# Kernel optimization log

Measured on AMD Instinct MI355X. Metric: run time of the kernel, lower is better.

Reference implementation:

```python
import jax, jax.numpy as jnp
import numpy as np

KEY_DIM = 32
NUM_HEADS = 4
B, T, F, D = 32, 64, 128, 64


def _proj_in(x, w, b):
    # x: [B,T,F,D], w: [D,H,K], b: [H,K] -> [B,T,F,H,K]
    return jnp.einsum("btfd,dhk->btfhk", x, w) + b


def _axial_mha(x, wq, bq, wk, bk, wv, bv, wo, bo, axis):
    # Keras MultiHeadAttention with attention_axes=(axis,); dropout inactive at inference.
    scale = 1.0 / np.sqrt(KEY_DIM)
    q = _proj_in(x, wq, bq) * scale
    k = _proj_in(x, wk, bk)
    v = _proj_in(x, wv, bv)
    if axis == 1:  # temporal attention, feature axis acts as batch
        scores = jnp.einsum("bqfhk,bsfhk->bfhqs", q, k)  # [B,F,H,Tq,Tk]
        probs = jax.nn.softmax(scores, axis=-1)
        o = jnp.einsum("bfhqs,bsfhk->bqfhk", probs, v)
    else:  # feature attention, temporal axis acts as batch
        scores = jnp.einsum("btqhk,btshk->bthqs", q, k)  # [B,T,H,Fq,Fk]
        probs = jax.nn.softmax(scores, axis=-1)
        o = jnp.einsum("bthqs,btshk->btqhk", probs, v)
    return jnp.einsum("btfhk,hkd->btfd", o, wo) + bo


def setup_inputs() -> dict:
    key = jax.random.key(0)
    ks = jax.random.split(key, 10)
    std = 0.02
    w = lambda k, shape: (jax.random.normal(k, shape, jnp.float32) * std)
    inp = {"x": jax.random.normal(ks[0], (B, T, F, D), jnp.float32)}
    for i, n in enumerate(["tq", "tk", "tv", "fq", "fk", "fv"]):
        inp[n + "_w"] = w(ks[1 + i], (D, NUM_HEADS, KEY_DIM))
        inp[n + "_b"] = jnp.zeros((NUM_HEADS, KEY_DIM), jnp.float32)
    inp["to_w"] = w(ks[7], (NUM_HEADS, KEY_DIM, D))
    inp["to_b"] = jnp.zeros((D,), jnp.float32)
    inp["fo_w"] = w(ks[8], (NUM_HEADS, KEY_DIM, D))
    inp["fo_b"] = jnp.zeros((D,), jnp.float32)
    return inp


def reference(x, tq_w, tq_b, tk_w, tk_b, tv_w, tv_b, to_w, to_b,
              fq_w, fq_b, fk_w, fk_b, fv_w, fv_b, fo_w, fo_b):
    temporal_out = _axial_mha(x, tq_w, tq_b, tk_w, tk_b, tv_w, tv_b, to_w, to_b, axis=1)
    feature_out = _axial_mha(x, fq_w, fq_b, fk_w, fk_b, fv_w, fv_b, fo_w, fo_b, axis=2)
    return temporal_out + feature_out
```

## Files before the change

kernel.cpp:

```cpp
#include <hip/hip_runtime.h>

typedef unsigned short u16;
typedef unsigned int   u32;
typedef short v8s __attribute__((ext_vector_type(8)));
typedef float v4f __attribute__((ext_vector_type(4)));

#define DEV __device__ __forceinline__
#define MFMA(a,b,c) __builtin_amdgcn_mfma_f32_16x16x32_bf16((a),(b),(c),0,0,0)

constexpr int Bb = 32, Tt = 64, Ff = 128, Dd = 64, Hh = 4, Kk = 32;

DEV u16 f2b(float f) {
    u32 u = __float_as_uint(f);
    return (u16)((u + 0x7fffu + ((u >> 16) & 1u)) >> 16);
}

__global__ __launch_bounds__(256)
void prep_weights(const float* __restrict__ tq, const float* __restrict__ tk,
                  const float* __restrict__ tv, const float* __restrict__ fq,
                  const float* __restrict__ fk, const float* __restrict__ fv,
                  const float* __restrict__ to_, const float* __restrict__ fo,
                  u16* __restrict__ ws)
{
    int idx = blockIdx.x * 256 + threadIdx.x;
    if (idx < 49152) {
        int p = idx >> 13, rem = idx & 8191;
        int h = rem >> 11, ch = (rem >> 6) & 31, d = rem & 63;
        const float* w = (p==0)?tq:(p==1)?tk:(p==2)?tv:(p==3)?fq:(p==4)?fk:fv;
        ws[idx] = f2b(w[d*128 + h*32 + ch]);
    } else {
        int i2 = idx - 49152;
        int path = i2 >> 13, rem = i2 & 8191;
        int h = rem >> 11, d = (rem >> 5) & 63, k2 = rem & 31;
        const float* w = path ? fo : to_;
        ws[idx] = f2b(w[h*2048 + k2*64 + d]);
    }
}

template<int NR, int MODE>
__global__ __launch_bounds__(NR*4)
void axial_mfma(const float* __restrict__ x, const u16* __restrict__ wsw,
                const float* __restrict__ bq, const float* __restrict__ bk,
                const float* __restrict__ bv, const float* __restrict__ bo,
                float* __restrict__ out)
{
    constexpr int W   = NR / 16;
    constexpr int NT  = W * 64;
    constexpr int NRp = NR + 8;
    constexpr int o_ql = 0;
    constexpr int o_kl = o_ql + NR * 32;
    constexpr int o_vt = o_kl + NR * 32;
    constexpr int o_pl = o_vt + 32 * NRp;
    constexpr int SMEM = o_pl + NR * NRp;
    __shared__ alignas(16) u16 sm[SMEM];
    (void)NT;

    const int tid  = threadIdx.x;
    const int w    = tid >> 6;
    const int lane = tid & 63;
    const int quad = lane >> 4;
    const int l15  = lane & 15;
    const int bid  = blockIdx.x;

    int base, rstride;
    if (MODE == 0) { int b = bid >> 7, f = bid & 127; base = b*(Tt*Ff*Dd) + f*Dd; rstride = Ff*Dd; }
    else           { base = bid * (Ff*Dd); rstride = Dd; }

    constexpr int PB = (MODE == 0) ? 0 : 3;
    const u16* wql = wsw + (PB+0)*8192;
    const u16* wkl = wsw + (PB+1)*8192;
    const u16* wvl = wsw + (PB+2)*8192;
    const u16* wol = wsw + 49152 + MODE*8192;

    v8s xfrag[2];
#pragma unroll
    for (int ks = 0; ks < 2; ++ks) {
        const float* xp = x + base + (w*16 + l15)*rstride + ks*32 + quad*8;
        float4 a = *reinterpret_cast<const float4*>(xp);
        float4 b = *reinterpret_cast<const float4*>(xp + 4);
        v8s f;
        f[0]=(short)f2b(a.x); f[1]=(short)f2b(a.y); f[2]=(short)f2b(a.z); f[3]=(short)f2b(a.w);
        f[4]=(short)f2b(b.x); f[5]=(short)f2b(b.y); f[6]=(short)f2b(b.z); f[7]=(short)f2b(b.w);
        xfrag[ks] = f;
    }

    v4f outAcc[4];
#pragma unroll
    for (int i = 0; i < 4; ++i) outAcc[i] = (v4f){0.f,0.f,0.f,0.f};

    const float scale = 0.17677669529663687f;
    const v4f vzero = (v4f){0.f,0.f,0.f,0.f};

#pragma unroll 1
    for (int h = 0; h < Hh; ++h) {
        __syncthreads();

        {
            const u16* wb = wql + h*2048;
#pragma unroll
            for (int nt = 0; nt < 2; ++nt) {
                v4f acc = vzero;
#pragma unroll
                for (int ks = 0; ks < 2; ++ks) {
                    v8s wf = *reinterpret_cast<const v8s*>(wb + (nt*16+l15)*64 + ks*32 + quad*8);
                    acc = MFMA(xfrag[ks], wf, acc);
                }
                float bias = bq[h*32 + nt*16 + l15];
#pragma unroll
                for (int r = 0; r < 4; ++r)
                    sm[o_ql + (w*16 + quad*4 + r)*32 + nt*16 + l15] = f2b((acc[r] + bias) * scale);
            }
        }
        {
            const u16* wb = wkl + h*2048;
#pragma unroll
            for (int nt = 0; nt < 2; ++nt) {
                v4f acc = vzero;
#pragma unroll
                for (int ks = 0; ks < 2; ++ks) {
                    v8s wf = *reinterpret_cast<const v8s*>(wb + (nt*16+l15)*64 + ks*32 + quad*8);
                    acc = MFMA(xfrag[ks], wf, acc);
                }
                float bias = bk[h*32 + nt*16 + l15];
#pragma unroll
                for (int r = 0; r < 4; ++r)
                    sm[o_kl + (w*16 + quad*4 + r)*32 + nt*16 + l15] = f2b(acc[r] + bias);
            }
        }
        {
            const u16* wb = wvl + h*2048;
#pragma unroll
            for (int nt = 0; nt < 2; ++nt) {
                v4f acc = vzero;
#pragma unroll
                for (int ks = 0; ks < 2; ++ks) {
                    v8s wf = *reinterpret_cast<const v8s*>(wb + (nt*16+l15)*64 + ks*32 + quad*8);
                    acc = MFMA(xfrag[ks], wf, acc);
                }
                float bias = bv[h*32 + nt*16 + l15];
                u32 lo = (u32)f2b(acc[0]+bias) | ((u32)f2b(acc[1]+bias) << 16);
                u32 hi = (u32)f2b(acc[2]+bias) | ((u32)f2b(acc[3]+bias) << 16);
                int ch = nt*16 + l15;
                *reinterpret_cast<uint2*>(&sm[o_vt + ch*NRp + w*16 + quad*4]) = make_uint2(lo, hi);
            }
        }
        __syncthreads();

        v8s qf = *reinterpret_cast<const v8s*>(&sm[o_ql + (w*16 + l15)*32 + quad*8]);
        v4f S[W];
#pragma unroll
        for (int ct = 0; ct < W; ++ct) {
            v8s kf = *reinterpret_cast<const v8s*>(&sm[o_kl + (ct*16 + l15)*32 + quad*8]);
            S[ct] = MFMA(qf, kf, vzero);
        }
        float mrow[4], rl[4];
#pragma unroll
        for (int r = 0; r < 4; ++r) {
            float mm = S[0][r];
#pragma unroll
            for (int ct = 1; ct < W; ++ct) mm = fmaxf(mm, S[ct][r]);
#pragma unroll
            for (int msk = 1; msk < 16; msk <<= 1) mm = fmaxf(mm, __shfl_xor(mm, msk, 16));
            mrow[r] = mm;
        }
#pragma unroll
        for (int r = 0; r < 4; ++r) {
            float ss = 0.f;
#pragma unroll
            for (int ct = 0; ct < W; ++ct) { float p = __expf(S[ct][r] - mrow[r]); S[ct][r] = p; ss += p; }
#pragma unroll
            for (int msk = 1; msk < 16; msk <<= 1) ss += __shfl_xor(ss, msk, 16);
            rl[r] = 1.f / ss;
        }
#pragma unroll
        for (int ct = 0; ct < W; ++ct)
#pragma unroll
            for (int r = 0; r < 4; ++r)
                sm[o_pl + (w*16 + quad*4 + r)*NRp + ct*16 + l15] = f2b(S[ct][r] * rl[r]);

        v4f Oacc[2] = { vzero, vzero };
#pragma unroll
        for (int ks = 0; ks < NR/32; ++ks) {
            v8s pf = *reinterpret_cast<const v8s*>(&sm[o_pl + (w*16 + l15)*NRp + ks*32 + quad*8]);
#pragma unroll
            for (int nt = 0; nt < 2; ++nt) {
                v8s vf = *reinterpret_cast<const v8s*>(&sm[o_vt + (nt*16 + l15)*NRp + ks*32 + quad*8]);
                Oacc[nt] = MFMA(pf, vf, Oacc[nt]);
            }
        }
#pragma unroll
        for (int nt = 0; nt < 2; ++nt)
#pragma unroll
            for (int r = 0; r < 4; ++r)
                sm[o_ql + (w*16 + quad*4 + r)*32 + nt*16 + l15] = f2b(Oacc[nt][r]);

        v8s of = *reinterpret_cast<const v8s*>(&sm[o_ql + (w*16 + l15)*32 + quad*8]);
        {
            const u16* wb = wol + h*2048;
#pragma unroll
            for (int nt = 0; nt < 4; ++nt) {
                v8s wf = *reinterpret_cast<const v8s*>(wb + (nt*16 + l15)*32 + quad*8);
                outAcc[nt] = MFMA(of, wf, outAcc[nt]);
            }
        }
    }

#pragma unroll
    for (int nt = 0; nt < 4; ++nt) {
        int d = nt*16 + l15;
        float bias = bo[d];
#pragma unroll
        for (int r = 0; r < 4; ++r) {
            int row = w*16 + quad*4 + r;
            float* p = out + base + row*rstride + d;
            float v = outAcc[nt][r] + bias;
            if (MODE == 1) v += *p;
            *p = v;
        }
    }
}

extern "C" void kernel_launch(void* const* d_in, const int* in_sizes, int n_in,
                              void* d_out, int out_size, void* d_ws, size_t ws_size,
                              hipStream_t stream) {
    const float* x   = (const float*)d_in[0];
    const float* tqw = (const float*)d_in[1];  const float* tqb = (const float*)d_in[2];
    const float* tkw = (const float*)d_in[3];  const float* tkb = (const float*)d_in[4];
    const float* tvw = (const float*)d_in[5];  const float* tvb = (const float*)d_in[6];
    const float* fqw = (const float*)d_in[7];  const float* fqb = (const float*)d_in[8];
    const float* fkw = (const float*)d_in[9];  const float* fkb = (const float*)d_in[10];
    const float* fvw = (const float*)d_in[11]; const float* fvb = (const float*)d_in[12];
    const float* tow = (const float*)d_in[13]; const float* tob = (const float*)d_in[14];
    const float* fow = (const float*)d_in[15]; const float* fob = (const float*)d_in[16];
    float* out = (float*)d_out;
    u16* ws = (u16*)d_ws;

    hipLaunchKernelGGL(prep_weights, dim3(256), dim3(256), 0, stream,
                       tqw, tkw, tvw, fqw, fkw, fvw, tow, fow, ws);
    hipLaunchKernelGGL((axial_mfma<64,0>), dim3(Bb*Ff), dim3(256), 0, stream,
                       x, ws, tqb, tkb, tvb, tob, out);
    hipLaunchKernelGGL((axial_mfma<128,1>), dim3(Bb*Tt), dim3(512), 0, stream,
                       x, ws, fqb, fkb, fvb, fob, out);
}
```

Measured before the change: 390.8 us.

## Transpose MFMA operand order for packed stores, row-local softmax, and vectorized output

Swaps the A/B operands of the Q, K, score, PV and output-projection MFMAs so each lane holds four consecutive columns of a single row. This lets the kernel write bf16 pairs with packed 64-bit LDS stores and float4 global stores instead of scalar ones. Softmax now reduces across quads with two cross-lane shuffles instead of four, and the Q/K LDS rows are padded to 40 elements to reduce bank conflicts. It also replaces the round-to-nearest-even bf16 conversion with a cheaper round-half-up packed conversion, which changes rounding slightly.

Result: faster. 381.0 us (-2.5%).

```diff
diff --git a/kernel.cpp b/kernel.cpp
--- a/kernel.cpp
+++ b/kernel.cpp
@@ -13,6 +13,11 @@
 DEV u16 f2b(float f) {
     u32 u = __float_as_uint(f);
     return (u16)((u + 0x7fffu + ((u >> 16) & 1u)) >> 16);
+}
+DEV u32 pk2(float a, float b) {
+    u32 x = __float_as_uint(a) + 0x8000u;
+    u32 y = __float_as_uint(b) + 0x8000u;
+    return (x >> 16) | (y & 0xffff0000u);
 }
 
 __global__ __launch_bounds__(256)
@@ -45,15 +50,14 @@
                 float* __restrict__ out)
 {
     constexpr int W   = NR / 16;
-    constexpr int NT  = W * 64;
+    constexpr int QP  = 40;
     constexpr int NRp = NR + 8;
-    constexpr int o_ql = 0;
-    constexpr int o_kl = o_ql + NR * 32;
-    constexpr int o_vt = o_kl + NR * 32;
-    constexpr int o_pl = o_vt + 32 * NRp;
-    constexpr int SMEM = o_pl + NR * NRp;
+    constexpr int o_q  = 0;
+    constexpr int o_k  = o_q + NR * QP;
+    constexpr int o_vt = o_k + NR * QP;
+    constexpr int o_p  = o_vt + 32 * NRp;
+    constexpr int SMEM = o_p + NR * NRp;
     __shared__ alignas(16) u16 sm[SMEM];
-    (void)NT;
 
     const int tid  = threadIdx.x;
     const int w    = tid >> 6;
@@ -79,8 +83,9 @@
         float4 a = *reinterpret_cast<const float4*>(xp);
         float4 b = *reinterpret_cast<const float4*>(xp + 4);
         v8s f;
-        f[0]=(short)f2b(a.x); f[1]=(short)f2b(a.y); f[2]=(short)f2b(a.z); f[3]=(short)f2b(a.w);
-        f[4]=(short)f2b(b.x); f[5]=(short)f2b(b.y); f[6]=(short)f2b(b.z); f[7]=(short)f2b(b.w);
+        u32* fu = reinterpret_cast<u32*>(&f);
+        fu[0] = pk2(a.x, a.y); fu[1] = pk2(a.z, a.w);
+        fu[2] = pk2(b.x, b.y); fu[3] = pk2(b.z, b.w);
         xfrag[ks] = f;
     }
 
@@ -103,12 +108,12 @@
 #pragma unroll
                 for (int ks = 0; ks < 2; ++ks) {
                     v8s wf = *reinterpret_cast<const v8s*>(wb + (nt*16+l15)*64 + ks*32 + quad*8);
-                    acc = MFMA(xfrag[ks], wf, acc);
+                    acc = MFMA(wf, xfrag[ks], acc);
                 }
-                float bias = bq[h*32 + nt*16 + l15];
-#pragma unroll
-                for (int r = 0; r < 4; ++r)
-                    sm[o_ql + (w*16 + quad*4 + r)*32 + nt*16 + l15] = f2b((acc[r] + bias) * scale);
+                float4 b4 = *reinterpret_cast<const float4*>(bq + h*32 + nt*16 + quad*4);
+                u32 lo = pk2((acc[0]+b4.x)*scale, (acc[1]+b4.y)*scale);
+                u32 hi = pk2((acc[2]+b4.z)*scale, (acc[3]+b4.w)*scale);
+                *reinterpret_cast<uint2*>(&sm[o_q + (w*16+l15)*QP + nt*16 + quad*4]) = make_uint2(lo, hi);
             }
         }
         {
@@ -119,12 +124,12 @@
 #pragma unroll
                 for (int ks = 0; ks < 2; ++ks) {
                     v8s wf = *reinterpret_cast<const v8s*>(wb + (nt*16+l15)*64 + ks*32 + quad*8);
-                    acc = MFMA(xfrag[ks], wf, acc);
+                    acc = MFMA(wf, xfrag[ks], acc);
                 }
-                float bias = bk[h*32 + nt*16 + l15];
-#pragma unroll
-                for (int r = 0; r < 4; ++r)
-                    sm[o_kl + (w*16 + quad*4 + r)*32 + nt*16 + l15] = f2b(acc[r] + bias);
+                float4 b4 = *reinterpret_cast<const float4*>(bk + h*32 + nt*16 + quad*4);
+                u32 lo = pk2(acc[0]+b4.x, acc[1]+b4.y);
+                u32 hi = pk2(acc[2]+b4.z, acc[3]+b4.w);
+                *reinterpret_cast<uint2*>(&sm[o_k + (w*16+l15)*QP + nt*16 + quad*4]) = make_uint2(lo, hi);
             }
         }
         {
@@ -138,85 +143,83 @@
                     acc = MFMA(xfrag[ks], wf, acc);
                 }
                 float bias = bv[h*32 + nt*16 + l15];
-                u32 lo = (u32)f2b(acc[0]+bias) | ((u32)f2b(acc[1]+bias) << 16);
-                u32 hi = (u32)f2b(acc[2]+bias) | ((u32)f2b(acc[3]+bias) << 16);
+                u32 lo = pk2(acc[0]+bias, acc[1]+bias);
+                u32 hi = pk2(acc[2]+bias, acc[3]+bias);
                 int ch = nt*16 + l15;
                 *reinterpret_cast<uint2*>(&sm[o_vt + ch*NRp + w*16 + quad*4]) = make_uint2(lo, hi);
             }
         }
         __syncthreads();
 
-        v8s qf = *reinterpret_cast<const v8s*>(&sm[o_ql + (w*16 + l15)*32 + quad*8]);
+        v8s qf = *reinterpret_cast<const v8s*>(&sm[o_q + (w*16+l15)*QP + quad*8]);
         v4f S[W];
 #pragma unroll
         for (int ct = 0; ct < W; ++ct) {
-            v8s kf = *reinterpret_cast<const v8s*>(&sm[o_kl + (ct*16 + l15)*32 + quad*8]);
-            S[ct] = MFMA(qf, kf, vzero);
-        }
-        float mrow[4], rl[4];
-#pragma unroll
-        for (int r = 0; r < 4; ++r) {
-            float mm = S[0][r];
-#pragma unroll
-            for (int ct = 1; ct < W; ++ct) mm = fmaxf(mm, S[ct][r]);
-#pragma unroll
-            for (int msk = 1; msk < 16; msk <<= 1) mm = fmaxf(mm, __shfl_xor(mm, msk, 16));
-            mrow[r] = mm;
-        }
-#pragma unroll
-        for (int r = 0; r < 4; ++r) {
-            float ss = 0.f;
-#pragma unroll
-            for (int ct = 0; ct < W; ++ct) { float p = __expf(S[ct][r] - mrow[r]); S[ct][r] = p; ss += p; }
-#pragma unroll
-            for (int msk = 1; msk < 16; msk <<= 1) ss += __shfl_xor(ss, msk, 16);
-            rl[r] = 1.f / ss;
-        }
+            v8s kf = *reinterpret_cast<const v8s*>(&sm[o_k + (ct*16+l15)*QP + quad*8]);
+            S[ct] = MFMA(kf, qf, vzero);
+        }
+        float mm = S[0][0];
 #pragma unroll
         for (int ct = 0; ct < W; ++ct)
 #pragma unroll
-            for (int r = 0; r < 4; ++r)
-                sm[o_pl + (w*16 + quad*4 + r)*NRp + ct*16 + l15] = f2b(S[ct][r] * rl[r]);
+            for (int r = 0; r < 4; ++r) mm = fmaxf(mm, S[ct][r]);
+        mm = fmaxf(mm, __shfl_xor(mm, 16));
+        mm = fmaxf(mm, __shfl_xor(mm, 32));
+        float ss = 0.f;
+#pragma unroll
+        for (int ct = 0; ct < W; ++ct)
+#pragma unroll
+            for (int r = 0; r < 4; ++r) { float p = __expf(S[ct][r] - mm); S[ct][r] = p; ss += p; }
+        ss += __shfl_xor(ss, 16);
+        ss += __shfl_xor(ss, 32);
+        float rl = 1.f / ss;
+#pragma unroll
+        for (int ct = 0; ct < W; ++ct) {
+            u32 lo = pk2(S[ct][0]*rl, S[ct][1]*rl);
+            u32 hi = pk2(S[ct][2]*rl, S[ct][3]*rl);
+            *reinterpret_cast<uint2*>(&sm[o_p + (w*16+l15)*NRp + ct*16 + quad*4]) = make_uint2(lo, hi);
+        }
 
         v4f Oacc[2] = { vzero, vzero };
 #pragma unroll
         for (int ks = 0; ks < NR/32; ++ks) {
-            v8s pf = *reinterpret_cast<const v8s*>(&sm[o_pl + (w*16 + l15)*NRp + ks*32 + quad*8]);
-#pragma unroll
-            for (int nt = 0; nt < 2; ++nt) {
-                v8s vf = *reinterpret_cast<const v8s*>(&sm[o_vt + (nt*16 + l15)*NRp + ks*32 + quad*8]);
-                Oacc[nt] = MFMA(pf, vf, Oacc[nt]);
-            }
-        }
-#pragma unroll
-        for (int nt = 0; nt < 2; ++nt)
-#pragma unroll
-            for (int r = 0; r < 4; ++r)
-                sm[o_ql + (w*16 + quad*4 + r)*32 + nt*16 + l15] = f2b(Oacc[nt][r]);
-
-        v8s of = *reinterpret_cast<const v8s*>(&sm[o_ql + (w*16 + l15)*32 + quad*8]);
+            v8s pf = *reinterpret_cast<const v8s*>(&sm[o_p + (w*16+l15)*NRp + ks*32 + quad*8]);
+#pragma unroll
+            for (int nt = 0; nt < 2; ++nt) {
+                v8s vf = *reinterpret_cast<const v8s*>(&sm[o_vt + (nt*16+l15)*NRp + ks*32 + quad*8]);
+                Oacc[nt] = MFMA(vf, pf, Oacc[nt]);
+            }
+        }
+#pragma unroll
+        for (int nt = 0; nt < 2; ++nt) {
+            u32 lo = pk2(Oacc[nt][0], Oacc[nt][1]);
+            u32 hi = pk2(Oacc[nt][2], Oacc[nt][3]);
+            *reinterpret_cast<uint2*>(&sm[o_q + (w*16+l15)*QP + nt*16 + quad*4]) = make_uint2(lo, hi);
+        }
+
+        v8s of = *reinterpret_cast<const v8s*>(&sm[o_q + (w*16+l15)*QP + quad*8]);
         {
             const u16* wb = wol + h*2048;
 #pragma unroll
             for (int nt = 0; nt < 4; ++nt) {
-                v8s wf = *reinterpret_cast<const v8s*>(wb + (nt*16 + l15)*32 + quad*8);
-                outAcc[nt] = MFMA(of, wf, outAcc[nt]);
-            }
-        }
-    }
-
+                v8s wf = *reinterpret_cast<const v8s*>(wb + (nt*16+l15)*32 + quad*8);
+                outAcc[nt] = MFMA(wf, of, outAcc[nt]);
+            }
+        }
+    }
+
+    float* orow = out + base + (w*16 + l15)*rstride;
 #pragma unroll
     for (int nt = 0; nt < 4; ++nt) {
-        int d = nt*16 + l15;
-        float bias = bo[d];
-#pragma unroll
-        for (int r = 0; r < 4; ++r) {
-            int row = w*16 + quad*4 + r;
-            float* p = out + base + row*rstride + d;
-            float v = outAcc[nt][r] + bias;
-            if (MODE == 1) v += *p;
-            *p = v;
-        }
+        int d0 = nt*16 + quad*4;
+        float4 b4 = *reinterpret_cast<const float4*>(bo + d0);
+        float4 v = make_float4(outAcc[nt][0]+b4.x, outAcc[nt][1]+b4.y,
+                               outAcc[nt][2]+b4.z, outAcc[nt][3]+b4.w);
+        if (MODE == 1) {
+            float4 p = *reinterpret_cast<const float4*>(orow + d0);
+            v.x += p.x; v.y += p.y; v.z += p.z; v.w += p.w;
+        }
+        *reinterpret_cast<float4*>(orow + d0) = v;
     }
 }
 
```
